# Performance work log

Measured on AMD Instinct MI355X. Metric: run time of the kernel, lower is better.

The kernel has to match this reference:

```python
import jax, jax.numpy as jnp
import numpy as np

N_ENT = 50000
N_REL = 200
DIM = 128
N_BASES = 4
NUM_RELATIONS = 2 * N_REL  # RGCNConv num_relations
E = 200000
S = 20000


def rgcn_conv(x, edge_index, edge_type, edge_norm, basis, att, root, bias, n_nodes):
    """RGCNConv with basis decomposition, aggr='mean'.
    x: [N, Din]; basis: [B, Din, Dout]; att: [R, B]; root: [Din, Dout]; bias: [Dout].
    """
    src, dst = edge_index[0], edge_index[1]
    x_j = x[src]                      # [E, Din] gather
    att_e = att[edge_type]            # [E, B]
    # message: x_j @ (att_e @ basis) without materializing per-edge [Din,Dout] weights
    msg = jnp.einsum('ei,bio,eb->eo', x_j, basis, att_e)  # [E, Dout]
    msg = msg * edge_norm[:, None]
    agg = jax.ops.segment_sum(msg, dst, num_segments=n_nodes)            # [N, Dout]
    cnt = jax.ops.segment_sum(jnp.ones_like(edge_norm), dst, num_segments=n_nodes)
    agg = agg / jnp.maximum(cnt, 1.0)[:, None]            # mean aggregation
    return agg + x @ root + bias


def setup_inputs() -> dict:
    key = jax.random.key(0)
    ks = jax.random.split(key, 20)
    d = {}
    d['entity'] = jnp.arange(N_ENT, dtype=jnp.int64) if jax.config.read('jax_enable_x64') else jnp.arange(N_ENT, dtype=jnp.int32)
    d['edge_index'] = jax.random.randint(ks[0], (2, E), 0, N_ENT)
    d['edge_type'] = jax.random.randint(ks[1], (E,), 0, NUM_RELATIONS)
    d['edge_norm'] = jax.random.uniform(ks[2], (E,), dtype=jnp.float32)
    d['samples'] = jax.random.randint(ks[3], (S, 3), 0, N_REL)
    d['DAD_rel'] = jax.random.normal(ks[4], (N_REL, N_REL), dtype=jnp.float32) * 0.05
    # learned parameters
    d['entity_emb'] = jax.random.normal(ks[5], (N_ENT, DIM), dtype=jnp.float32) * 0.02
    d['relation_emb'] = jax.random.normal(ks[6], (N_REL, DIM), dtype=jnp.float32) * 0.02
    d['entity_context_tab'] = jax.random.normal(ks[7], (N_ENT, DIM), dtype=jnp.float32) * 0.02
    d['relation_context_tab'] = jax.random.normal(ks[8], (N_REL, DIM), dtype=jnp.float32) * 0.02
    d['relation_gcn_weight'] = jax.random.normal(ks[9], (DIM, DIM), dtype=jnp.float32) * 0.02
    d['gate_entity'] = jax.random.uniform(ks[10], (DIM,), dtype=jnp.float32)
    d['gate_relation'] = jax.random.uniform(ks[11], (DIM,), dtype=jnp.float32)
    d['basis1'] = jax.random.normal(ks[12], (N_BASES, DIM, DIM), dtype=jnp.float32) * 0.02
    d['att1'] = jax.random.normal(ks[13], (NUM_RELATIONS, N_BASES), dtype=jnp.float32) * 0.1
    d['root1'] = jax.random.normal(ks[14], (DIM, DIM), dtype=jnp.float32) * 0.02
    d['bias1'] = jnp.zeros((DIM,), dtype=jnp.float32)
    d['basis2'] = jax.random.normal(ks[15], (N_BASES, DIM, DIM), dtype=jnp.float32) * 0.02
    d['att2'] = jax.random.normal(ks[16], (NUM_RELATIONS, N_BASES), dtype=jnp.float32) * 0.1
    d['root2'] = jax.random.normal(ks[17], (DIM, DIM), dtype=jnp.float32) * 0.02
    d['bias2'] = jnp.zeros((DIM,), dtype=jnp.float32)
    return d


def reference(entity, edge_index, edge_type, edge_norm, samples, DAD_rel,
              entity_emb, relation_emb, entity_context_tab, relation_context_tab,
              relation_gcn_weight, gate_entity, gate_relation,
              basis1, att1, root1, bias1, basis2, att2, root2, bias2):
    n_nodes = entity.shape[0]
    ent_ctx = entity_context_tab[entity]                  # [N, D]
    rel_ctx = relation_context_tab                        # arange over all relations -> full table
    ent_ctx = jax.nn.relu(rgcn_conv(ent_ctx, edge_index, edge_type, edge_norm,
                                    basis1, att1, root1, bias1, n_nodes))
    ent_ctx = jax.nn.relu(rgcn_conv(ent_ctx, edge_index, edge_type, edge_norm,
                                    basis2, att2, root2, bias2, n_nodes))
    rel_ctx = jax.nn.relu((DAD_rel @ rel_ctx) @ relation_gcn_weight)
    ge = jax.nn.sigmoid(gate_entity)
    gr = jax.nn.sigmoid(gate_relation)
    h, r, t = samples[:, 0], samples[:, 1], samples[:, 2]
    head_o = ge * entity_emb[h] + (1.0 - ge) * ent_ctx[h]
    rel_o = gr * relation_emb[r] + (1.0 - gr) * rel_ctx[r]
    tail_o = ge * entity_emb[t] + (1.0 - ge) * ent_ctx[t]
    return jnp.stack([head_o, rel_o, tail_o])             # [3, S, D]
```

## Files before the change

### kernel.cpp

```cpp
#include <hip/hip_runtime.h>
#include <hip/hip_bf16.h>

typedef short s8v  __attribute__((ext_vector_type(8)));
typedef float f4v  __attribute__((ext_vector_type(4)));
typedef float f16v __attribute__((ext_vector_type(16)));
typedef unsigned short us8 __attribute__((ext_vector_type(8)));

__device__ __forceinline__ unsigned short f2bf(float x) {
    unsigned u = __float_as_uint(x);
    unsigned r = ((u >> 16) & 1u) + 0x7FFFu;
    return (unsigned short)((u + r) >> 16);
}
__device__ __forceinline__ float bf2f(unsigned short h) {
    return __uint_as_float(((unsigned)h) << 16);
}

__global__ __launch_bounds__(256) void x0_kernel(
    const float* __restrict__ tab, const int* __restrict__ entity,
    float* __restrict__ X0, int N)
{
    int idx = blockIdx.x * 256 + threadIdx.x;
    int n = idx >> 5, l = idx & 31;
    if (n < N) {
        int src = entity[n];
        *(float4*)&X0[(size_t)n * 128 + l * 4] =
            *(const float4*)&tab[(size_t)src * 128 + l * 4];
    }
}

__global__ __launch_bounds__(256) void bprep_kernel(
    const float* __restrict__ basis1, const float* __restrict__ root1,
    const float* __restrict__ basis2, const float* __restrict__ root2,
    unsigned short* __restrict__ Bt1h, unsigned short* __restrict__ Bt1l,
    unsigned short* __restrict__ Bt2h, unsigned short* __restrict__ Bt2l)
{
    int idx = blockIdx.x * 256 + threadIdx.x;
    int layer = blockIdx.y;
    int n = idx & 127, k = idx >> 7;
    const float* basis = layer ? basis2 : basis1;
    const float* root  = layer ? root2  : root1;
    float v = (k < 512) ? basis[((k & 3) << 14) + ((k >> 2) << 7) + n]
                        : root[((k - 512) << 7) + n];
    unsigned short h = f2bf(v);
    unsigned short l = f2bf(v - bf2f(h));
    unsigned short* Bh = layer ? Bt2h : Bt1h;
    unsigned short* Bl = layer ? Bt2l : Bt1l;
    Bh[(size_t)n * 640 + k] = h;
    Bl[(size_t)n * 640 + k] = l;
}

__global__ __launch_bounds__(256) void hist_kernel(
    const int* __restrict__ edge_index, int* __restrict__ deg, int E)
{
    int e = blockIdx.x * 256 + threadIdx.x;
    if (e < E) atomicAdd(&deg[edge_index[E + e]], 1);
}

__global__ __launch_bounds__(1024) void scanA_kernel(
    const int* __restrict__ deg, int* __restrict__ row_start,
    int* __restrict__ btot, int N)
{
    __shared__ int wtot[16];
    __shared__ int woff[16];
    const int tid = threadIdx.x, lane = tid & 63, wid = tid >> 6;
    int i = blockIdx.x * 1024 + tid;
    int v = (i < N) ? deg[i] : 0;
    int x = v;
    #pragma unroll
    for (int d = 1; d < 64; d <<= 1) {
        int t = __shfl_up(x, d, 64);
        if (lane >= d) x += t;
    }
    if (lane == 63) wtot[wid] = x;
    __syncthreads();
    if (wid == 0 && lane < 16) {
        int s = wtot[lane];
        int y = s;
        #pragma unroll
        for (int d = 1; d < 16; d <<= 1) {
            int t = __shfl_up(y, d, 16);
            if (lane >= d) y += t;
        }
        woff[lane] = y - s;
        if (lane == 15) btot[blockIdx.x] = y;
    }
    __syncthreads();
    if (i < N) row_start[i] = woff[wid] + (x - v);
}

__global__ __launch_bounds__(64) void scanB_kernel(
    const int* __restrict__ btot, int* __restrict__ boff,
    int* __restrict__ row_start, int nB, int N)
{
    int t = threadIdx.x;
    int v = (t < nB) ? btot[t] : 0;
    int x = v;
    #pragma unroll
    for (int d = 1; d < 64; d <<= 1) {
        int u = __shfl_up(x, d, 64);
        if (t >= d) x += u;
    }
    if (t < nB) boff[t] = x - v;
    if (t == nB - 1) row_start[N] = x;
}

__global__ __launch_bounds__(1024) void scanC_kernel(
    int* __restrict__ row_start, int* __restrict__ cursor,
    const int* __restrict__ boff, int N)
{
    int i = blockIdx.x * 1024 + threadIdx.x;
    if (i < N) {
        int r = row_start[i] + boff[blockIdx.x];
        row_start[i] = r;
        cursor[i]    = r;
    }
}

__global__ __launch_bounds__(256) void fill_kernel(
    const int* __restrict__ edge_index, const int* __restrict__ edge_type,
    const float* __restrict__ edge_norm, int* __restrict__ cursor,
    int* __restrict__ src_s, int* __restrict__ et_s, float* __restrict__ norm_s, int E)
{
    int e = blockIdx.x * 256 + threadIdx.x;
    if (e >= E) return;
    int dst = edge_index[E + e];
    int pos = atomicAdd(&cursor[dst], 1);
    src_s[pos]  = edge_index[e];
    et_s[pos]   = edge_type[e];
    norm_s[pos] = edge_norm[e];
}

__global__ __launch_bounds__(256) void edge_agg_kernel(
    const float* __restrict__ X,
    const int* __restrict__ row_start,
    const int* __restrict__ src_s, const int* __restrict__ et_s,
    const float* __restrict__ norm_s,
    const float* __restrict__ att,
    unsigned short* __restrict__ w, int N)
{
    int n = blockIdx.x * 8 + (threadIdx.x >> 5);
    if (n >= N) return;
    int l = threadIdx.x & 31;
    int s0 = row_start[n], s1 = row_start[n + 1];
    float acc[4][4];
    #pragma unroll
    for (int d = 0; d < 4; ++d)
        #pragma unroll
        for (int b = 0; b < 4; ++b) acc[d][b] = 0.f;
    for (int p = s0; p < s1; ++p) {
        int   src  = src_s[p];
        int   et   = et_s[p];
        float norm = norm_s[p];
        float4 a = *(const float4*)(att + (size_t)et * 4);
        a.x *= norm; a.y *= norm; a.z *= norm; a.w *= norm;
        float4 x = *(const float4*)&X[(size_t)src * 128 + (l << 2)];
        float xs[4] = {x.x, x.y, x.z, x.w};
        #pragma unroll
        for (int d = 0; d < 4; ++d) {
            acc[d][0] = fmaf(a.x, xs[d], acc[d][0]);
            acc[d][1] = fmaf(a.y, xs[d], acc[d][1]);
            acc[d][2] = fmaf(a.z, xs[d], acc[d][2]);
            acc[d][3] = fmaf(a.w, xs[d], acc[d][3]);
        }
    }
    float inv = 1.0f / fmaxf((float)(s1 - s0), 1.0f);
    #pragma unroll
    for (int d = 0; d < 4; ++d) {
        ushort4 h;
        h.x = f2bf(acc[d][0] * inv);
        h.y = f2bf(acc[d][1] * inv);
        h.z = f2bf(acc[d][2] * inv);
        h.w = f2bf(acc[d][3] * inv);
        *(ushort4*)&w[(size_t)n * 512 + (l << 4) + (d << 2)] = h;
    }
}

__global__ __launch_bounds__(256) void gemm640_kernel(
    const unsigned short* __restrict__ wbf,
    const float* __restrict__ X,
    const unsigned short* __restrict__ Bth,
    const unsigned short* __restrict__ Btl,
    const float* __restrict__ bias,
    float* __restrict__ Xout, int N)
{
    __shared__ unsigned short A_hi[64 * 40];
    __shared__ unsigned short A_lo[64 * 40];
    __shared__ unsigned short B_hi[128 * 40];
    __shared__ unsigned short B_lo[128 * 40];

    const int tid  = threadIdx.x;
    const int row0 = blockIdx.x * 64;
    const int lane = tid & 63, wv = tid >> 6;
    const int m    = lane & 31;
    const int kh   = (lane >> 5) << 3;
    const int rt   = (wv & 1) << 5;
    const int c0w  = (wv >> 1) << 6;

    const int awr = tid >> 2, awk = (tid & 3) << 3;
    const int bn0 = tid >> 2,          bk0 = (tid & 3) << 3;
    const int bn1 = (tid + 256) >> 2,  bk1 = ((tid + 256) & 3) << 3;

    const us8 z8 = {0,0,0,0,0,0,0,0};
    us8 pA = z8, pBh0, pBh1, pBl0, pBl1;

    auto loadAw = [&](int k0) {
        int gr = row0 + awr;
        pA = (gr < N) ? *(const us8*)&wbf[(size_t)gr * 512 + k0 + awk] : z8;
    };
    auto loadB = [&](int k0) {
        pBh0 = *(const us8*)&Bth[(size_t)bn0 * 640 + k0 + bk0];
        pBh1 = *(const us8*)&Bth[(size_t)bn1 * 640 + k0 + bk1];
        pBl0 = *(const us8*)&Btl[(size_t)bn0 * 640 + k0 + bk0];
        pBl1 = *(const us8*)&Btl[(size_t)bn1 * 640 + k0 + bk1];
    };

    f16v acc0, acc1;
    #pragma unroll
    for (int i = 0; i < 16; ++i) { acc0[i] = 0.f; acc1[i] = 0.f; }

    loadAw(0); loadB(0);

    for (int kc = 0; kc < 20; ++kc) {
        const int k0 = kc * 32;
        if (kc) __syncthreads();

        if (k0 < 512) {
            *(us8*)&A_hi[awr * 40 + awk] = pA;
        } else {
            #pragma unroll
            for (int i = 0; i < 2; ++i) {
                int idx = tid + i * 256;
                int r = idx >> 3, kv = (idx & 7) << 2;
                int gr = row0 + r;
                float4 v = make_float4(0.f, 0.f, 0.f, 0.f);
                if (gr < N) v = *(const float4*)&X[(size_t)gr * 128 + (k0 - 512) + kv];
                ushort4 h, l;
                h.x = f2bf(v.x); l.x = f2bf(v.x - bf2f(h.x));
                h.y = f2bf(v.y); l.y = f2bf(v.y - bf2f(h.y));
                h.z = f2bf(v.z); l.z = f2bf(v.z - bf2f(h.z));
                h.w = f2bf(v.w); l.w = f2bf(v.w - bf2f(h.w));
                *(ushort4*)&A_hi[r * 40 + kv] = h;
                *(ushort4*)&A_lo[r * 40 + kv] = l;
            }
        }
        *(us8*)&B_hi[bn0 * 40 + bk0] = pBh0;
        *(us8*)&B_hi[bn1 * 40 + bk1] = pBh1;
        *(us8*)&B_lo[bn0 * 40 + bk0] = pBl0;
        *(us8*)&B_lo[bn1 * 40 + bk1] = pBl1;
        __syncthreads();

        if (kc < 19) {
            if (k0 + 32 < 512) loadAw(k0 + 32);
            loadB(k0 + 32);
        }

        #pragma unroll
        for (int h = 0; h < 2; ++h) {
            const int off = h * 16 + kh;
            s8v aH = *(const s8v*)&A_hi[(rt + m) * 40 + off];
            if (k0 < 512) {
                {
                    const int nb = (c0w + m) * 40 + off;
                    s8v bH = *(const s8v*)&B_hi[nb];
                    s8v bL = *(const s8v*)&B_lo[nb];
                    acc0 = __builtin_amdgcn_mfma_f32_32x32x16_bf16(aH, bL, acc0, 0, 0, 0);
                    acc0 = __builtin_amdgcn_mfma_f32_32x32x16_bf16(aH, bH, acc0, 0, 0, 0);
                }
                {
                    const int nb = (c0w + 32 + m) * 40 + off;
                    s8v bH = *(const s8v*)&B_hi[nb];
                    s8v bL = *(const s8v*)&B_lo[nb];
                    acc1 = __builtin_amdgcn_mfma_f32_32x32x16_bf16(aH, bL, acc1, 0, 0, 0);
                    acc1 = __builtin_amdgcn_mfma_f32_32x32x16_bf16(aH, bH, acc1, 0, 0, 0);
                }
            } else {
                s8v aL = *(const s8v*)&A_lo[(rt + m) * 40 + off];
                {
                    const int nb = (c0w + m) * 40 + off;
                    s8v bH = *(const s8v*)&B_hi[nb];
                    s8v bL = *(const s8v*)&B_lo[nb];
                    acc0 = __builtin_amdgcn_mfma_f32_32x32x16_bf16(aL, bH, acc0, 0, 0, 0);
                    acc0 = __builtin_amdgcn_mfma_f32_32x32x16_bf16(aH, bL, acc0, 0, 0, 0);
                    acc0 = __builtin_amdgcn_mfma_f32_32x32x16_bf16(aH, bH, acc0, 0, 0, 0);
                }
                {
                    const int nb = (c0w + 32 + m) * 40 + off;
                    s8v bH = *(const s8v*)&B_hi[nb];
                    s8v bL = *(const s8v*)&B_lo[nb];
                    acc1 = __builtin_amdgcn_mfma_f32_32x32x16_bf16(aL, bH, acc1, 0, 0, 0);
                    acc1 = __builtin_amdgcn_mfma_f32_32x32x16_bf16(aH, bL, acc1, 0, 0, 0);
                    acc1 = __builtin_amdgcn_mfma_f32_32x32x16_bf16(aH, bH, acc1, 0, 0, 0);
                }
            }
        }
    }

    const int rbase = rt + ((lane >> 5) << 2);
    #pragma unroll
    for (int ct = 0; ct < 2; ++ct) {
        int gc = c0w + ct * 32 + m;
        float bv = bias[gc];
        #pragma unroll
        for (int reg = 0; reg < 16; ++reg) {
            int gr = row0 + rbase + (reg & 3) + ((reg >> 2) << 3);
            if (gr < N) {
                float v = ct ? acc1[reg] : acc0[reg];
                Xout[(size_t)gr * 128 + gc] = fmaxf(v + bv, 0.f);
            }
        }
    }
}

__global__ __launch_bounds__(512) void relctx_kernel(
    const float* __restrict__ DAD,
    const float* __restrict__ tab,
    const float* __restrict__ W,
    float* __restrict__ R2, int NR)
{
    __shared__ float part[4][128];
    __shared__ float r1s[128];
    int r = blockIdx.x;
    int t = threadIdx.x;
    int o = t & 127, q = t >> 7;
    float s = 0.f;
    #pragma unroll 4
    for (int j = q; j < NR; j += 4)
        s = fmaf(DAD[r * NR + j], tab[j * 128 + o], s);
    part[q][o] = s;
    __syncthreads();
    if (t < 128) r1s[t] = part[0][t] + part[1][t] + part[2][t] + part[3][t];
    __syncthreads();
    float s2 = 0.f;
    #pragma unroll 8
    for (int k = q * 32; k < q * 32 + 32; ++k)
        s2 = fmaf(r1s[k], W[k * 128 + o], s2);
    part[q][o] = s2;
    __syncthreads();
    if (t < 128)
        R2[r * 128 + t] = fmaxf(part[0][t] + part[1][t] + part[2][t] + part[3][t], 0.f);
}

__global__ __launch_bounds__(256) void output_kernel(
    const int* __restrict__ samples,
    const float* __restrict__ gate_e,
    const float* __restrict__ gate_r,
    const float* __restrict__ ent_emb,
    const float* __restrict__ rel_emb,
    const float* __restrict__ ctx2,
    const float* __restrict__ relctx,
    float* __restrict__ out, int S)
{
    int s = blockIdx.x * 2 + (threadIdx.x >> 7);
    if (s >= S) return;
    int p = blockIdx.y;
    int o = threadIdx.x & 127;
    float v;
    if (p == 1) {
        int idx = samples[s * 3 + 1];
        float g = 1.0f / (1.0f + __expf(-gate_r[o]));
        v = g * rel_emb[idx * 128 + o] + (1.0f - g) * relctx[idx * 128 + o];
    } else {
        int idx = samples[s * 3 + (p == 0 ? 0 : 2)];
        float g = 1.0f / (1.0f + __expf(-gate_e[o]));
        v = g * ent_emb[(size_t)idx * 128 + o] + (1.0f - g) * ctx2[(size_t)idx * 128 + o];
    }
    out[(size_t)p * S * 128 + (size_t)s * 128 + o] = v;
}

extern "C" void kernel_launch(void* const* d_in, const int* in_sizes, int n_in,
                              void* d_out, int out_size, void* d_ws, size_t ws_size,
                              hipStream_t stream)
{
    const int*   entity     = (const int*)d_in[0];
    const int*   edge_index = (const int*)d_in[1];
    const int*   edge_type  = (const int*)d_in[2];
    const float* edge_norm  = (const float*)d_in[3];
    const int*   samples    = (const int*)d_in[4];
    const float* DAD        = (const float*)d_in[5];
    const float* ent_emb    = (const float*)d_in[6];
    const float* rel_emb    = (const float*)d_in[7];
    const float* ent_tab    = (const float*)d_in[8];
    const float* rel_tab    = (const float*)d_in[9];
    const float* Wrel       = (const float*)d_in[10];
    const float* gate_e     = (const float*)d_in[11];
    const float* gate_r     = (const float*)d_in[12];
    const float* basis1     = (const float*)d_in[13];
    const float* att1       = (const float*)d_in[14];
    const float* root1      = (const float*)d_in[15];
    const float* bias1      = (const float*)d_in[16];
    const float* basis2     = (const float*)d_in[17];
    const float* att2       = (const float*)d_in[18];
    const float* root2      = (const float*)d_in[19];
    const float* bias2      = (const float*)d_in[20];

    const int N  = in_sizes[0];
    const int E  = in_sizes[2];
    const int S  = in_sizes[4] / 3;
    const int NR = in_sizes[9] / 128;

    float* ws      = (float*)d_ws;
    float* X0      = ws;
    float* X1      = X0 + (size_t)N * 128;
    unsigned short* wbf = (unsigned short*)(X1 + (size_t)N * 128);
    float* Rc      = (float*)(wbf + (size_t)N * 512);
    int*   deg     = (int*)(Rc + (size_t)NR * 128);
    int*   rstart  = deg + N;
    int*   cursor  = rstart + N + 1;
    int*   src_s   = cursor + N;
    int*   et_s    = src_s + E;
    float* norm_s  = (float*)(et_s + E);
    int*   btot    = (int*)(norm_s + E);
    int*   boff    = btot + 64;
    uintptr_t bt   = ((uintptr_t)(boff + 64) + 15) & ~(uintptr_t)15;
    unsigned short* Bt1h = (unsigned short*)bt;
    unsigned short* Bt1l = Bt1h + 128 * 640;
    unsigned short* Bt2h = Bt1l + 128 * 640;
    unsigned short* Bt2l = Bt2h + 128 * 640;

    const int egrid = (E + 255) / 256;
    const int ggrid = (N + 63) / 64;
    const int agrid = (N + 7) / 8;
    const int nB    = (N + 1023) / 1024;

    bprep_kernel<<<dim3(320, 2), 256, 0, stream>>>(basis1, root1, basis2, root2,
                                                   Bt1h, Bt1l, Bt2h, Bt2l);
    hipMemsetAsync(deg, 0, (size_t)N * sizeof(int), stream);
    hist_kernel<<<egrid, 256, 0, stream>>>(edge_index, deg, E);
    scanA_kernel<<<nB, 1024, 0, stream>>>(deg, rstart, btot, N);
    scanB_kernel<<<1, 64, 0, stream>>>(btot, boff, rstart, nB, N);
    scanC_kernel<<<nB, 1024, 0, stream>>>(rstart, cursor, boff, N);
    fill_kernel<<<egrid, 256, 0, stream>>>(edge_index, edge_type, edge_norm, cursor,
                                           src_s, et_s, norm_s, E);

    x0_kernel<<<(N * 32 + 255) / 256, 256, 0, stream>>>(ent_tab, entity, X0, N);

    edge_agg_kernel<<<agrid, 256, 0, stream>>>(X0, rstart, src_s, et_s, norm_s, att1, wbf, N);
    gemm640_kernel<<<ggrid, 256, 0, stream>>>(wbf, X0, Bt1h, Bt1l, bias1, X1, N);

    edge_agg_kernel<<<agrid, 256, 0, stream>>>(X1, rstart, src_s, et_s, norm_s, att2, wbf, N);
    gemm640_kernel<<<ggrid, 256, 0, stream>>>(wbf, X1, Bt2h, Bt2l, bias2, X0, N);

    relctx_kernel<<<NR, 512, 0, stream>>>(DAD, rel_tab, Wrel, Rc, NR);

    output_kernel<<<dim3((S + 1) / 2, 3), 256, 0, stream>>>(
        samples, gate_e, gate_r, ent_emb, rel_emb, X0, Rc, (float*)d_out, S);
}
```

Measured before the change: 347.9 us.

## Precompute per-edge att*norm, unroll edge gather by 4, load GEMM B directly to registers

The fill kernel now multiplies att1/att2 rows by edge_norm per edge and stores them as float4 arrays, so the aggregation kernels no longer do the indirect att lookup. The edge aggregation loop processes four edges per iteration, clamping indices and zeroing weights past the row end, to expose more independent gathers. The GEMM's B operand is pre-packed into MFMA-fragment order and read straight from global memory into double-buffered registers, which drops the B shared-memory tiles and their stores. This costs extra workspace for the per-edge float4 arrays and more registers in the GEMM.

New measurement: 348.2 us. Within noise of the previous version (+0.1%).

```diff
diff --git a/kernel.cpp b/kernel.cpp
--- a/kernel.cpp
+++ b/kernel.cpp
@@ -2,9 +2,7 @@
 #include <hip/hip_bf16.h>
 
 typedef short s8v  __attribute__((ext_vector_type(8)));
-typedef float f4v  __attribute__((ext_vector_type(4)));
 typedef float f16v __attribute__((ext_vector_type(16)));
-typedef unsigned short us8 __attribute__((ext_vector_type(8)));
 
 __device__ __forceinline__ unsigned short f2bf(float x) {
     unsigned u = __float_as_uint(x);
@@ -31,8 +29,8 @@
 __global__ __launch_bounds__(256) void bprep_kernel(
     const float* __restrict__ basis1, const float* __restrict__ root1,
     const float* __restrict__ basis2, const float* __restrict__ root2,
-    unsigned short* __restrict__ Bt1h, unsigned short* __restrict__ Bt1l,
-    unsigned short* __restrict__ Bt2h, unsigned short* __restrict__ Bt2l)
+    unsigned short* __restrict__ Bp1h, unsigned short* __restrict__ Bp1l,
+    unsigned short* __restrict__ Bp2h, unsigned short* __restrict__ Bp2l)
 {
     int idx = blockIdx.x * 256 + threadIdx.x;
     int layer = blockIdx.y;
@@ -43,10 +41,11 @@
                         : root[((k - 512) << 7) + n];
     unsigned short h = f2bf(v);
     unsigned short l = f2bf(v - bf2f(h));
-    unsigned short* Bh = layer ? Bt2h : Bt1h;
-    unsigned short* Bl = layer ? Bt2l : Bt1l;
-    Bh[(size_t)n * 640 + k] = h;
-    Bl[(size_t)n * 640 + k] = l;
+    size_t pos = (((size_t)(k >> 3) * 128) + n) * 8 + (k & 7);
+    unsigned short* Bh = layer ? Bp2h : Bp1h;
+    unsigned short* Bl = layer ? Bp2l : Bp1l;
+    Bh[pos] = h;
+    Bl[pos] = l;
 }
 
 __global__ __launch_bounds__(256) void hist_kernel(
@@ -119,23 +118,27 @@
 __global__ __launch_bounds__(256) void fill_kernel(
     const int* __restrict__ edge_index, const int* __restrict__ edge_type,
     const float* __restrict__ edge_norm, int* __restrict__ cursor,
-    int* __restrict__ src_s, int* __restrict__ et_s, float* __restrict__ norm_s, int E)
+    const float* __restrict__ att1, const float* __restrict__ att2,
+    int* __restrict__ src_s, float4* __restrict__ an1, float4* __restrict__ an2, int E)
 {
     int e = blockIdx.x * 256 + threadIdx.x;
     if (e >= E) return;
     int dst = edge_index[E + e];
+    int et  = edge_type[e];
+    float n = edge_norm[e];
     int pos = atomicAdd(&cursor[dst], 1);
-    src_s[pos]  = edge_index[e];
-    et_s[pos]   = edge_type[e];
-    norm_s[pos] = edge_norm[e];
+    src_s[pos] = edge_index[e];
+    float4 a1 = *(const float4*)&att1[(size_t)et * 4];
+    float4 a2 = *(const float4*)&att2[(size_t)et * 4];
+    an1[pos] = make_float4(n * a1.x, n * a1.y, n * a1.z, n * a1.w);
+    an2[pos] = make_float4(n * a2.x, n * a2.y, n * a2.z, n * a2.w);
 }
 
 __global__ __launch_bounds__(256) void edge_agg_kernel(
     const float* __restrict__ X,
     const int* __restrict__ row_start,
-    const int* __restrict__ src_s, const int* __restrict__ et_s,
-    const float* __restrict__ norm_s,
-    const float* __restrict__ att,
+    const int* __restrict__ src_s,
+    const float4* __restrict__ an,
     unsigned short* __restrict__ w, int N)
 {
     int n = blockIdx.x * 8 + (threadIdx.x >> 5);
@@ -147,20 +150,32 @@
     for (int d = 0; d < 4; ++d)
         #pragma unroll
         for (int b = 0; b < 4; ++b) acc[d][b] = 0.f;
-    for (int p = s0; p < s1; ++p) {
-        int   src  = src_s[p];
-        int   et   = et_s[p];
-        float norm = norm_s[p];
-        float4 a = *(const float4*)(att + (size_t)et * 4);
-        a.x *= norm; a.y *= norm; a.z *= norm; a.w *= norm;
-        float4 x = *(const float4*)&X[(size_t)src * 128 + (l << 2)];
-        float xs[4] = {x.x, x.y, x.z, x.w};
+
+    for (int p = s0; p < s1; p += 4) {
+        int i1 = min(p + 1, s1 - 1);
+        int i2 = min(p + 2, s1 - 1);
+        int i3 = min(p + 3, s1 - 1);
+        int sA = src_s[p],  sB = src_s[i1];
+        int sC = src_s[i2], sD = src_s[i3];
+        float4 aA = an[p],  aB = an[i1];
+        float4 aC = an[i2], aD = an[i3];
+        if (p + 1 >= s1) aB = make_float4(0.f, 0.f, 0.f, 0.f);
+        if (p + 2 >= s1) aC = make_float4(0.f, 0.f, 0.f, 0.f);
+        if (p + 3 >= s1) aD = make_float4(0.f, 0.f, 0.f, 0.f);
+        float4 xA = *(const float4*)&X[(size_t)sA * 128 + (l << 2)];
+        float4 xB = *(const float4*)&X[(size_t)sB * 128 + (l << 2)];
+        float4 xC = *(const float4*)&X[(size_t)sC * 128 + (l << 2)];
+        float4 xD = *(const float4*)&X[(size_t)sD * 128 + (l << 2)];
+        float xsA[4] = {xA.x, xA.y, xA.z, xA.w};
+        float xsB[4] = {xB.x, xB.y, xB.z, xB.w};
+        float xsC[4] = {xC.x, xC.y, xC.z, xC.w};
+        float xsD[4] = {xD.x, xD.y, xD.z, xD.w};
         #pragma unroll
         for (int d = 0; d < 4; ++d) {
-            acc[d][0] = fmaf(a.x, xs[d], acc[d][0]);
-            acc[d][1] = fmaf(a.y, xs[d], acc[d][1]);
-            acc[d][2] = fmaf(a.z, xs[d], acc[d][2]);
-            acc[d][3] = fmaf(a.w, xs[d], acc[d][3]);
+            acc[d][0] = fmaf(aA.x, xsA[d], fmaf(aB.x, xsB[d], fmaf(aC.x, xsC[d], fmaf(aD.x, xsD[d], acc[d][0]))));
+            acc[d][1] = fmaf(aA.y, xsA[d], fmaf(aB.y, xsB[d], fmaf(aC.y, xsC[d], fmaf(aD.y, xsD[d], acc[d][1]))));
+            acc[d][2] = fmaf(aA.z, xsA[d], fmaf(aB.z, xsB[d], fmaf(aC.z, xsC[d], fmaf(aD.z, xsD[d], acc[d][2]))));
+            acc[d][3] = fmaf(aA.w, xsA[d], fmaf(aB.w, xsB[d], fmaf(aC.w, xsC[d], fmaf(aD.w, xsD[d], acc[d][3]))));
         }
     }
     float inv = 1.0f / fmaxf((float)(s1 - s0), 1.0f);
@@ -178,124 +193,112 @@
 __global__ __launch_bounds__(256) void gemm640_kernel(
     const unsigned short* __restrict__ wbf,
     const float* __restrict__ X,
-    const unsigned short* __restrict__ Bth,
-    const unsigned short* __restrict__ Btl,
+    const unsigned short* __restrict__ Bph,
+    const unsigned short* __restrict__ Bpl,
     const float* __restrict__ bias,
     float* __restrict__ Xout, int N)
 {
     __shared__ unsigned short A_hi[64 * 40];
     __shared__ unsigned short A_lo[64 * 40];
-    __shared__ unsigned short B_hi[128 * 40];
-    __shared__ unsigned short B_lo[128 * 40];
 
     const int tid  = threadIdx.x;
     const int row0 = blockIdx.x * 64;
     const int lane = tid & 63, wv = tid >> 6;
     const int m    = lane & 31;
-    const int kh   = (lane >> 5) << 3;
+    const int kh8  = lane >> 5;
     const int rt   = (wv & 1) << 5;
     const int c0w  = (wv >> 1) << 6;
 
-    const int awr = tid >> 2, awk = (tid & 3) << 3;
-    const int bn0 = tid >> 2,          bk0 = (tid & 3) << 3;
-    const int bn1 = (tid + 256) >> 2,  bk1 = ((tid + 256) & 3) << 3;
-
-    const us8 z8 = {0,0,0,0,0,0,0,0};
-    us8 pA = z8, pBh0, pBh1, pBl0, pBl1;
-
-    auto loadAw = [&](int k0) {
-        int gr = row0 + awr;
-        pA = (gr < N) ? *(const us8*)&wbf[(size_t)gr * 512 + k0 + awk] : z8;
+    const int ar  = tid >> 2;
+    const int akv = (tid & 3) << 3;
+
+    const s8v z8 = {0,0,0,0,0,0,0,0};
+    s8v pA = z8;
+    float4 pX0, pX1;
+    s8v B0[8], B1[8];
+
+    auto loadB = [&](int kc, s8v (&dst)[8]) {
+        #pragma unroll
+        for (int h = 0; h < 2; ++h) {
+            int khg = kc * 4 + h * 2 + kh8;
+            #pragma unroll
+            for (int ct = 0; ct < 2; ++ct) {
+                size_t off = ((size_t)khg * 128 + (c0w + ct * 32 + m)) * 8;
+                dst[h * 4 + ct * 2 + 0] = *(const s8v*)&Bph[off];
+                dst[h * 4 + ct * 2 + 1] = *(const s8v*)&Bpl[off];
+            }
+        }
     };
-    auto loadB = [&](int k0) {
-        pBh0 = *(const us8*)&Bth[(size_t)bn0 * 640 + k0 + bk0];
-        pBh1 = *(const us8*)&Bth[(size_t)bn1 * 640 + k0 + bk1];
-        pBl0 = *(const us8*)&Btl[(size_t)bn0 * 640 + k0 + bk0];
-        pBl1 = *(const us8*)&Btl[(size_t)bn1 * 640 + k0 + bk1];
+    auto loadA = [&](int kc) {
+        int k0 = kc * 32;
+        int gr = row0 + ar;
+        if (k0 < 512) {
+            pA = (gr < N) ? *(const s8v*)&wbf[(size_t)gr * 512 + k0 + akv] : z8;
+        } else {
+            pX0 = make_float4(0.f, 0.f, 0.f, 0.f);
+            pX1 = pX0;
+            if (gr < N) {
+                pX0 = *(const float4*)&X[(size_t)gr * 128 + (k0 - 512) + akv];
+                pX1 = *(const float4*)&X[(size_t)gr * 128 + (k0 - 512) + akv + 4];
+            }
+        }
     };
 
     f16v acc0, acc1;
     #pragma unroll
     for (int i = 0; i < 16; ++i) { acc0[i] = 0.f; acc1[i] = 0.f; }
 
-    loadAw(0); loadB(0);
-
-    for (int kc = 0; kc < 20; ++kc) {
+    loadA(0);
+    loadB(0, B0);
+
+    auto chunk = [&](int kc, s8v (&cur)[8], s8v (&nxt)[8]) {
         const int k0 = kc * 32;
         if (kc) __syncthreads();
-
         if (k0 < 512) {
-            *(us8*)&A_hi[awr * 40 + awk] = pA;
+            *(s8v*)&A_hi[ar * 40 + akv] = pA;
         } else {
+            float f[8] = {pX0.x, pX0.y, pX0.z, pX0.w, pX1.x, pX1.y, pX1.z, pX1.w};
+            s8v h8, l8;
             #pragma unroll
-            for (int i = 0; i < 2; ++i) {
-                int idx = tid + i * 256;
-                int r = idx >> 3, kv = (idx & 7) << 2;
-                int gr = row0 + r;
-                float4 v = make_float4(0.f, 0.f, 0.f, 0.f);
-                if (gr < N) v = *(const float4*)&X[(size_t)gr * 128 + (k0 - 512) + kv];
-                ushort4 h, l;
-                h.x = f2bf(v.x); l.x = f2bf(v.x - bf2f(h.x));
-                h.y = f2bf(v.y); l.y = f2bf(v.y - bf2f(h.y));
-                h.z = f2bf(v.z); l.z = f2bf(v.z - bf2f(h.z));
-                h.w = f2bf(v.w); l.w = f2bf(v.w - bf2f(h.w));
-                *(ushort4*)&A_hi[r * 40 + kv] = h;
-                *(ushort4*)&A_lo[r * 40 + kv] = l;
+            for (int j = 0; j < 8; ++j) {
+                unsigned short h = f2bf(f[j]);
+                h8[j] = (short)h;
+                l8[j] = (short)f2bf(f[j] - bf2f(h));
             }
-        }
-        *(us8*)&B_hi[bn0 * 40 + bk0] = pBh0;
-        *(us8*)&B_hi[bn1 * 40 + bk1] = pBh1;
-        *(us8*)&B_lo[bn0 * 40 + bk0] = pBl0;
-        *(us8*)&B_lo[bn1 * 40 + bk1] = pBl1;
+            *(s8v*)&A_hi[ar * 40 + akv] = h8;
+            *(s8v*)&A_lo[ar * 40 + akv] = l8;
+        }
         __syncthreads();
-
-        if (kc < 19) {
-            if (k0 + 32 < 512) loadAw(k0 + 32);
-            loadB(k0 + 32);
-        }
+        if (kc < 19) { loadA(kc + 1); loadB(kc + 1, nxt); }
 
         #pragma unroll
         for (int h = 0; h < 2; ++h) {
-            const int off = h * 16 + kh;
+            const int off = h * 16 + kh8 * 8;
             s8v aH = *(const s8v*)&A_hi[(rt + m) * 40 + off];
             if (k0 < 512) {
-                {
-                    const int nb = (c0w + m) * 40 + off;
-                    s8v bH = *(const s8v*)&B_hi[nb];
-                    s8v bL = *(const s8v*)&B_lo[nb];
-                    acc0 = __builtin_amdgcn_mfma_f32_32x32x16_bf16(aH, bL, acc0, 0, 0, 0);
-                    acc0 = __builtin_amdgcn_mfma_f32_32x32x16_bf16(aH, bH, acc0, 0, 0, 0);
-                }
-                {
-                    const int nb = (c0w + 32 + m) * 40 + off;
-                    s8v bH = *(const s8v*)&B_hi[nb];
-                    s8v bL = *(const s8v*)&B_lo[nb];
-                    acc1 = __builtin_amdgcn_mfma_f32_32x32x16_bf16(aH, bL, acc1, 0, 0, 0);
-                    acc1 = __builtin_amdgcn_mfma_f32_32x32x16_bf16(aH, bH, acc1, 0, 0, 0);
-                }
+                acc0 = __builtin_amdgcn_mfma_f32_32x32x16_bf16(aH, cur[h*4+1], acc0, 0, 0, 0);
+                acc0 = __builtin_amdgcn_mfma_f32_32x32x16_bf16(aH, cur[h*4+0], acc0, 0, 0, 0);
+                acc1 = __builtin_amdgcn_mfma_f32_32x32x16_bf16(aH, cur[h*4+3], acc1, 0, 0, 0);
+                acc1 = __builtin_amdgcn_mfma_f32_32x32x16_bf16(aH, cur[h*4+2], acc1, 0, 0, 0);
             } else {
                 s8v aL = *(const s8v*)&A_lo[(rt + m) * 40 + off];
-                {
-                    const int nb = (c0w + m) * 40 + off;
-                    s8v bH = *(const s8v*)&B_hi[nb];
-                    s8v bL = *(const s8v*)&B_lo[nb];
-                    acc0 = __builtin_amdgcn_mfma_f32_32x32x16_bf16(aL, bH, acc0, 0, 0, 0);
-                    acc0 = __builtin_amdgcn_mfma_f32_32x32x16_bf16(aH, bL, acc0, 0, 0, 0);
-                    acc0 = __builtin_amdgcn_mfma_f32_32x32x16_bf16(aH, bH, acc0, 0, 0, 0);
-                }
-                {
-                    const int nb = (c0w + 32 + m) * 40 + off;
-                    s8v bH = *(const s8v*)&B_hi[nb];
-                    s8v bL = *(const s8v*)&B_lo[nb];
-                    acc1 = __builtin_amdgcn_mfma_f32_32x32x16_bf16(aL, bH, acc1, 0, 0, 0);
-                    acc1 = __builtin_amdgcn_mfma_f32_32x32x16_bf16(aH, bL, acc1, 0, 0, 0);
-                    acc1 = __builtin_amdgcn_mfma_f32_32x32x16_bf16(aH, bH, acc1, 0, 0, 0);
-                }
+                acc0 = __builtin_amdgcn_mfma_f32_32x32x16_bf16(aL, cur[h*4+0], acc0, 0, 0, 0);
+                acc0 = __builtin_amdgcn_mfma_f32_32x32x16_bf16(aH, cur[h*4+1], acc0, 0, 0, 0);
+                acc0 = __builtin_amdgcn_mfma_f32_32x32x16_bf16(aH, cur[h*4+0], acc0, 0, 0, 0);
+                acc1 = __builtin_amdgcn_mfma_f32_32x32x16_bf16(aL, cur[h*4+2], acc1, 0, 0, 0);
+                acc1 = __builtin_amdgcn_mfma_f32_32x32x16_bf16(aH, cur[h*4+3], acc1, 0, 0, 0);
+                acc1 = __builtin_amdgcn_mfma_f32_32x32x16_bf16(aH, cur[h*4+2], acc1, 0, 0, 0);
             }
         }
-    }
-
-    const int rbase = rt + ((lane >> 5) << 2);
+    };
+
+    #pragma unroll 1
+    for (int kc2 = 0; kc2 < 10; ++kc2) {
+        chunk(kc2 * 2,     B0, B1);
+        chunk(kc2 * 2 + 1, B1, B0);
+    }
+
+    const int rbase = rt + (kh8 << 2);
     #pragma unroll
     for (int ct = 0; ct < 2; ++ct) {
         int gc = c0w + ct * 32 + m;
@@ -401,21 +404,21 @@
     float* ws      = (float*)d_ws;
     float* X0      = ws;
     float* X1      = X0 + (size_t)N * 128;
-    unsigned short* wbf = (unsigned short*)(X1 + (size_t)N * 128);
+    float4* an1    = (float4*)(X1 + (size_t)N * 128);
+    float4* an2    = an1 + (E + 4);
+    unsigned short* wbf = (unsigned short*)(an2 + (E + 4));
     float* Rc      = (float*)(wbf + (size_t)N * 512);
     int*   deg     = (int*)(Rc + (size_t)NR * 128);
     int*   rstart  = deg + N;
     int*   cursor  = rstart + N + 1;
     int*   src_s   = cursor + N;
-    int*   et_s    = src_s + E;
-    float* norm_s  = (float*)(et_s + E);
-    int*   btot    = (int*)(norm_s + E);
+    int*   btot    = src_s + E + 4;
     int*   boff    = btot + 64;
     uintptr_t bt   = ((uintptr_t)(boff + 64) + 15) & ~(uintptr_t)15;
-    unsigned short* Bt1h = (unsigned short*)bt;
-    unsigned short* Bt1l = Bt1h + 128 * 640;
-    unsigned short* Bt2h = Bt1l + 128 * 640;
-    unsigned short* Bt2l = Bt2h + 128 * 640;
+    unsigned short* Bp1h = (unsigned short*)bt;
+    unsigned short* Bp1l = Bp1h + 80 * 128 * 8;
+    unsigned short* Bp2h = Bp1l + 80 * 128 * 8;
+    unsigned short* Bp2l = Bp2h + 80 * 128 * 8;
 
     const int egrid = (E + 255) / 256;
     const int ggrid = (N + 63) / 64;
@@ -423,22 +426,22 @@
     const int nB    = (N + 1023) / 1024;
 
     bprep_kernel<<<dim3(320, 2), 256, 0, stream>>>(basis1, root1, basis2, root2,
-                                                   Bt1h, Bt1l, Bt2h, Bt2l);
+                                                   Bp1h, Bp1l, Bp2h, Bp2l);
     hipMemsetAsync(deg, 0, (size_t)N * sizeof(int), stream);
     hist_kernel<<<egrid, 256, 0, stream>>>(edge_index, deg, E);
     scanA_kernel<<<nB, 1024, 0, stream>>>(deg, rstart, btot, N);
     scanB_kernel<<<1, 64, 0, stream>>>(btot, boff, rstart, nB, N);
     scanC_kernel<<<nB, 1024, 0, stream>>>(rstart, cursor, boff, N);
     fill_kernel<<<egrid, 256, 0, stream>>>(edge_index, edge_type, edge_norm, cursor,
-                                           src_s, et_s, norm_s, E);
+                                           att1, att2, src_s, an1, an2, E);
 
     x0_kernel<<<(N * 32 + 255) / 256, 256, 0, stream>>>(ent_tab, entity, X0, N);
 
-    edge_agg_kernel<<<agrid, 256, 0, stream>>>(X0, rstart, src_s, et_s, norm_s, att1, wbf, N);
-    gemm640_kernel<<<ggrid, 256, 0, stream>>>(wbf, X0, Bt1h, Bt1l, bias1, X1, N);
-
-    edge_agg_kernel<<<agrid, 256, 0, stream>>>(X1, rstart, src_s, et_s, norm_s, att2, wbf, N);
-    gemm640_kernel<<<ggrid, 256, 0, stream>>>(wbf, X1, Bt2h, Bt2l, bias2, X0, N);
+    edge_agg_kernel<<<agrid, 256, 0, stream>>>(X0, rstart, src_s, an1, wbf, N);
+    gemm640_kernel<<<ggrid, 256, 0, stream>>>(wbf, X0, Bp1h, Bp1l, bias1, X1, N);
+
+    edge_agg_kernel<<<agrid, 256, 0, stream>>>(X1, rstart, src_s, an2, wbf, N);
+    gemm640_kernel<<<ggrid, 256, 0, stream>>>(wbf, X1, Bp2h, Bp2l, bias2, X0, N);
 
     relctx_kernel<<<NR, 512, 0, stream>>>(DAD, rel_tab, Wrel, Rc, NR);
 
```
